# Optimization experiments

Measured on AMD Instinct MI355X. Metric: run time of the kernel, lower is better.

## Reference

```python
import jax, jax.numpy as jnp
import numpy as np

B, NB, D, H = 16384, 3, 1024, 8
HD = D // H
EPS = 1e-5

def setup_inputs() -> dict:
    key = jax.random.key(0)
    ks = jax.random.split(key, 24)
    w = lambda k, shp: jax.random.normal(k, shp, jnp.float32) * 0.02
    return {
        "x": jax.random.normal(ks[0], (B, NB, D), jnp.float32),
        # nn.MultiheadAttention params
        "in_proj_w": w(ks[1], (3 * D, D)),
        "in_proj_b": jnp.zeros((3 * D,), jnp.float32),
        "out_w": w(ks[2], (D, D)),
        "out_b": jnp.zeros((D,), jnp.float32),
        # weight_generator MLP
        "wg1_w": w(ks[3], (D, D * NB)), "wg1_b": jnp.zeros((D,), jnp.float32),
        "wg2_w": w(ks[4], (D // 2, D)), "wg2_b": jnp.zeros((D // 2,), jnp.float32),
        "wg3_w": w(ks[5], (NB, D // 2)), "wg3_b": jnp.zeros((NB,), jnp.float32),
        # refiner MLP + LayerNorms
        "r1_w": w(ks[6], (2 * D, D)), "r1_b": jnp.zeros((2 * D,), jnp.float32),
        "ln1_g": jnp.ones((2 * D,), jnp.float32), "ln1_b": jnp.zeros((2 * D,), jnp.float32),
        "r2_w": w(ks[7], (D, 2 * D)), "r2_b": jnp.zeros((D,), jnp.float32),
        "ln2_g": jnp.ones((D,), jnp.float32), "ln2_b": jnp.zeros((D,), jnp.float32),
    }

def _layernorm(x, g, b):
    m = jnp.mean(x, axis=-1, keepdims=True)
    v = jnp.mean(jnp.square(x - m), axis=-1, keepdims=True)
    return (x - m) * jax.lax.rsqrt(v + EPS) * g + b

def _forward(x, in_proj_w, in_proj_b, out_w, out_b,
             wg1_w, wg1_b, wg2_w, wg2_b, wg3_w, wg3_b,
             r1_w, r1_b, ln1_g, ln1_b, r2_w, r2_b, ln2_g, ln2_b):
    b = x.shape[0]
    # --- cross (self) attention over the NB branch tokens ---
    qkv = jnp.einsum("bsd,ed->bse", x, in_proj_w) + in_proj_b  # [B, NB, 3D]
    q, k, v = jnp.split(qkv, 3, axis=-1)
    q = q.reshape(b, NB, H, HD)
    k = k.reshape(b, NB, H, HD)
    v = v.reshape(b, NB, H, HD)
    scores = jnp.einsum("bqhd,bkhd->bhqk", q, k) / jnp.sqrt(jnp.float32(HD))
    attn = jax.nn.softmax(scores, axis=-1)
    o = jnp.einsum("bhqk,bkhd->bqhd", attn, v).reshape(b, NB, D)
    attended = jnp.einsum("bsd,ed->bse", o, out_w) + out_b  # [B, NB, D]
    # --- dynamic softmax gate over branches ---
    flat = attended.reshape(b, NB * D)
    h = jax.nn.relu(flat @ wg1_w.T + wg1_b)
    h = jax.nn.relu(h @ wg2_w.T + wg2_b)
    weights = jax.nn.softmax(h @ wg3_w.T + wg3_b, axis=-1)  # [B, NB]
    weighted = jnp.einsum("bsd,bs->bd", attended, weights)  # [B, D]
    # --- refiner (dropout inactive in eval) ---
    h = weighted @ r1_w.T + r1_b
    h = jax.nn.relu(_layernorm(h, ln1_g, ln1_b))
    out = h @ r2_w.T + r2_b
    return _layernorm(out, ln2_g, ln2_b)

def reference(x, in_proj_w, in_proj_b, out_w, out_b,
              wg1_w, wg1_b, wg2_w, wg2_b, wg3_w, wg3_b,
              r1_w, r1_b, ln1_g, ln1_b, r2_w, r2_b, ln2_g, ln2_b):
    return _forward(x, in_proj_w, in_proj_b, out_w, out_b,
                    wg1_w, wg1_b, wg2_w, wg2_b, wg3_w, wg3_b,
                    r1_w, r1_b, ln1_g, ln1_b, r2_w, r2_b, ln2_g, ln2_b)
```

## Files before the change

### kernel.cpp

```cpp
#include <hip/hip_runtime.h>
#include <hip/hip_bf16.h>

#define BB   16384
#define NBR  3
#define DD   1024
#define HH   8
#define HDD  128

typedef __attribute__((ext_vector_type(8))) short short8;
typedef __attribute__((ext_vector_type(4))) float f32x4;

__device__ __forceinline__ float b2f(ushort u) {
    union { unsigned int i; float f; } x; x.i = ((unsigned int)u) << 16; return x.f;
}
__device__ __forceinline__ ushort f2b(float f) {
    union { __hip_bfloat16 h; ushort u; } x; x.h = __float2bfloat16(f); return x.u;
}

__global__ __launch_bounds__(256) void cvt_f32_bf16(const float* __restrict__ in,
                                                    ushort* __restrict__ out, long n) {
    long i = ((long)blockIdx.x * 256 + threadIdx.x) * 4;
    if (i + 4 > n) return;
    float4 v = *reinterpret_cast<const float4*>(in + i);
    unsigned int a = ((unsigned int)f2b(v.x)) | (((unsigned int)f2b(v.y)) << 16);
    unsigned int b = ((unsigned int)f2b(v.z)) | (((unsigned int)f2b(v.w)) << 16);
    uint2 p; p.x = a; p.y = b;
    *reinterpret_cast<uint2*>(out + i) = p;
}

template<int EPI>
__global__ __launch_bounds__(512, 2)
void gemm256(const ushort* __restrict__ A, const ushort* __restrict__ Bt,
             const float* __restrict__ bias, void* __restrict__ Cout,
             int M, int N, int K) {
    extern __shared__ ushort lds[];

    const int tid  = threadIdx.x;
    const int wid  = tid >> 6;
    const int lane = tid & 63;
    const int cpx  = gridDim.x >> 3;
    const int bid  = (blockIdx.x & 7) * cpx + (blockIdx.x >> 3);
    const int nbn  = N >> 8;
    const int bm   = bid / nbn;
    const int bn   = bid % nbn;
    const long m0  = (long)bm * 256;
    const long n0  = (long)bn * 256;
    const int NT   = K >> 6;

    const int srow = tid >> 3;
    const int kel  = (((tid & 7) ^ (srow & 7)) << 3);
    const int widEl = wid * 512;

    const ushort* gA[2][2];
    const ushort* gB[2][2];
    #pragma unroll
    for (int c = 0; c < 2; c++)
        #pragma unroll
        for (int j = 0; j < 2; j++) {
            gA[c][j] = A  + (size_t)(m0 + c * 128 + j * 64 + srow) * K + kel;
            gB[c][j] = Bt + (size_t)(n0 + c * 128 + j * 64 + srow) * K + kel;
        }

    const int wr = wid >> 2, wc = wid & 3;
    const int lm15 = lane & 15;
    int aoff[8];
    #pragma unroll
    for (int m = 0; m < 8; m++) aoff[m] = (wr * 128 + m * 16 + lm15) * 64;
    int boff[4];
    #pragma unroll
    for (int c = 0; c < 4; c++) boff[c] = (wc * 64 + c * 16 + lm15) * 64;
    const int kbr[2] = {
        (((0 << 6) | ((lane >> 4) << 4)) ^ ((lane & 7) << 4)) >> 1,
        (((1 << 6) | ((lane >> 4) << 4)) ^ ((lane & 7) << 4)) >> 1
    };

    f32x4 acc[8][4];
    #pragma unroll
    for (int m = 0; m < 8; m++)
        #pragma unroll
        for (int c = 0; c < 4; c++) { f32x4 z = {0.f, 0.f, 0.f, 0.f}; acc[m][c] = z; }

    short8 af[8], bf[2];

#define STAGE(C, PB, TT) { \
    const ushort* _g0; const ushort* _g1; int _b; \
    if ((C) < 2) { _g0 = gA[(C)][0] + (TT) * 64; _g1 = gA[(C)][1] + (TT) * 64; \
                   _b = (PB) * 16384 + (C) * 8192 + widEl; } \
    else         { _g0 = gB[(C) - 2][0] + (TT) * 64; _g1 = gB[(C) - 2][1] + (TT) * 64; \
                   _b = 32768 + (PB) * 16384 + ((C) - 2) * 8192 + widEl; } \
    __builtin_amdgcn_global_load_lds((const __attribute__((address_space(1))) void*)_g0, \
        (__attribute__((address_space(3))) void*)&lds[_b], 16, 0, 0); \
    __builtin_amdgcn_global_load_lds((const __attribute__((address_space(1))) void*)_g1, \
        (__attribute__((address_space(3))) void*)&lds[_b + 4096], 16, 0, 0); }

#define READ_A(P, KK) { \
    _Pragma("unroll") \
    for (int _m = 0; _m < 8; _m++) \
        af[_m] = *(const short8*)&lds[(P) * 16384 + aoff[_m] + kbr[KK]]; }

#define READ_B2(P, KK, C0) { \
    bf[0] = *(const short8*)&lds[32768 + (P) * 16384 + boff[(C0)] + kbr[KK]]; \
    bf[1] = *(const short8*)&lds[32768 + (P) * 16384 + boff[(C0) + 1] + kbr[KK]]; }

#define MFMA8x2(C0) { \
    _Pragma("unroll") \
    for (int _m = 0; _m < 8; _m++) { \
        acc[_m][(C0)]     = __builtin_amdgcn_mfma_f32_16x16x32_bf16(af[_m], bf[0], acc[_m][(C0)], 0, 0, 0); \
        acc[_m][(C0) + 1] = __builtin_amdgcn_mfma_f32_16x16x32_bf16(af[_m], bf[1], acc[_m][(C0) + 1], 0, 0, 0); } }

#define TILE_STEP(P, T, PRE) { \
     \
    if (PRE) STAGE(0, (P) ^ 1, (T) + 1); \
    if (PRE) { asm volatile("s_waitcnt vmcnt(2)" ::: "memory"); } \
    else     { asm volatile("s_waitcnt vmcnt(0)" ::: "memory"); } \
    __builtin_amdgcn_s_barrier(); \
    asm volatile("" ::: "memory"); \
    __builtin_amdgcn_sched_barrier(0); \
    READ_A(P, 0); \
    READ_B2(P, 0, 0); \
    __builtin_amdgcn_s_setprio(1); MFMA8x2(0); __builtin_amdgcn_s_setprio(0); \
    __builtin_amdgcn_s_barrier(); \
     \
    if (PRE) STAGE(1, (P) ^ 1, (T) + 1); \
    READ_B2(P, 0, 2); \
    __builtin_amdgcn_s_barrier(); \
    __builtin_amdgcn_s_setprio(1); MFMA8x2(2); __builtin_amdgcn_s_setprio(0); \
    __builtin_amdgcn_s_barrier(); \
     \
    if (PRE) STAGE(2, (P) ^ 1, (T) + 1); \
    READ_A(P, 1); \
    READ_B2(P, 1, 0); \
    __builtin_amdgcn_s_barrier(); \
    __builtin_amdgcn_s_setprio(1); MFMA8x2(0); __builtin_amdgcn_s_setprio(0); \
    __builtin_amdgcn_s_barrier(); \
     \
    if (PRE) STAGE(3, (P) ^ 1, (T) + 1); \
    READ_B2(P, 1, 2); \
    __builtin_amdgcn_s_barrier(); \
    __builtin_amdgcn_s_setprio(1); MFMA8x2(2); __builtin_amdgcn_s_setprio(0); \
    __builtin_amdgcn_s_barrier(); }

    STAGE(0, 0, 0); STAGE(1, 0, 0); STAGE(2, 0, 0); STAGE(3, 0, 0);

    int t = 0;
    for (; t + 2 < NT; t += 2) {
        TILE_STEP(0, t, true);
        TILE_STEP(1, t + 1, true);
    }
    TILE_STEP(0, t, true);
    TILE_STEP(1, t + 1, false);

#undef TILE_STEP
#undef MFMA8x2
#undef READ_B2
#undef READ_A
#undef STAGE

    const int l16 = lane >> 4;
    #pragma unroll
    for (int c = 0; c < 4; c++) {
        const long col = n0 + wc * 64 + c * 16 + lm15;
        const float bc = bias[col];
        #pragma unroll
        for (int m = 0; m < 8; m++) {
            const long row = m0 + wr * 128 + m * 16 + l16 * 4;
            #pragma unroll
            for (int j = 0; j < 4; j++) {
                float v = acc[m][c][j] + bc;
                if (EPI == 1) v = v > 0.f ? v : 0.f;
                if (EPI == 2) ((float*)Cout)[(row + j) * (long)N + col] = v;
                else          ((ushort*)Cout)[(row + j) * (long)N + col] = f2b(v);
            }
        }
    }
}

template<int EPI>
__global__ __launch_bounds__(256, 2)
void gemm_bt(const ushort* __restrict__ A, const ushort* __restrict__ Bt,
             const float* __restrict__ bias, void* __restrict__ Cout,
             int M, int N, int K) {
    __shared__ ushort As[128 * 64];
    __shared__ ushort Bs[128 * 64];
    const int tid  = threadIdx.x;
    const int wid  = tid >> 6;
    const int lane = tid & 63;
    const int cpx  = gridDim.x >> 3;
    const int bid  = (blockIdx.x & 7) * cpx + (blockIdx.x >> 3);
    const int nbn  = N >> 7;
    const int bm   = bid / nbn;
    const int bn   = bid % nbn;
    const long m0  = (long)bm * 128;
    const long n0  = (long)bn * 128;

    const int srow = tid >> 3;
    const int scol = (tid & 7) << 3;
    const ushort* gA = A  + (m0 + srow) * (long)K + scol;
    const ushort* gB = Bt + (n0 + srow) * (long)K + scol;

    f32x4 acc[4][4];
    #pragma unroll
    for (int i = 0; i < 4; i++)
        #pragma unroll
        for (int j = 0; j < 4; j++) { f32x4 z = {0.f, 0.f, 0.f, 0.f}; acc[i][j] = z; }

    const int wr = wid >> 1, wc = wid & 1;
    const int kits = K >> 6;

    for (int kt = 0; kt < kits; ++kt) {
        const ushort* pA = gA + kt * 64;
        const ushort* pB = gB + kt * 64;
        #pragma unroll
        for (int i = 0; i < 4; i++) {
            __builtin_amdgcn_global_load_lds(
                (const __attribute__((address_space(1))) void*)(pA + (long)i * 32 * K),
                (__attribute__((address_space(3))) void*)&As[(i * 32 + wid * 8) * 64],
                16, 0, 0);
        }
        #pragma unroll
        for (int i = 0; i < 4; i++) {
            __builtin_amdgcn_global_load_lds(
                (const __attribute__((address_space(1))) void*)(pB + (long)i * 32 * K),
                (__attribute__((address_space(3))) void*)&Bs[(i * 32 + wid * 8) * 64],
                16, 0, 0);
        }
        __syncthreads();
        #pragma unroll
        for (int kk = 0; kk < 2; kk++) {
            const int ko = kk * 32 + (lane >> 4) * 8;
            short8 af[4], bf[4];
            #pragma unroll
            for (int m = 0; m < 4; m++)
                af[m] = *(const short8*)&As[(wr * 64 + m * 16 + (lane & 15)) * 64 + ko];
            #pragma unroll
            for (int n = 0; n < 4; n++)
                bf[n] = *(const short8*)&Bs[(wc * 64 + n * 16 + (lane & 15)) * 64 + ko];
            #pragma unroll
            for (int m = 0; m < 4; m++)
                #pragma unroll
                for (int n = 0; n < 4; n++)
                    acc[m][n] = __builtin_amdgcn_mfma_f32_16x16x32_bf16(af[m], bf[n], acc[m][n], 0, 0, 0);
        }
        __syncthreads();
    }

    #pragma unroll
    for (int n = 0; n < 4; n++) {
        const long c = n0 + wc * 64 + n * 16 + (lane & 15);
        const float bc = bias[c];
        #pragma unroll
        for (int m = 0; m < 4; m++) {
            const long r = m0 + wr * 64 + m * 16 + (lane >> 4) * 4;
            #pragma unroll
            for (int j = 0; j < 4; j++) {
                float v = acc[m][n][j] + bc;
                if (EPI == 1) v = v > 0.f ? v : 0.f;
                if (EPI == 2) ((float*)Cout)[(r + j) * (long)N + c] = v;
                else          ((ushort*)Cout)[(r + j) * (long)N + c] = f2b(v);
            }
        }
    }
}

__global__ __launch_bounds__(256) void attn_kernel(const ushort* __restrict__ qkv,
                                                   ushort* __restrict__ o) {
    const int w    = (blockIdx.x * 256 + threadIdx.x) >> 6;
    const int lane = threadIdx.x & 63;
    const int b = w >> 3, h = w & 7;
    const ushort* base = qkv + (size_t)b * (3 * 3072) + h * HDD + lane * 2;

    float q[3][2], k[3][2], v[3][2];
    #pragma unroll
    for (int i = 0; i < 3; i++) {
        unsigned int qu = *(const unsigned int*)(base + i * 3072);
        unsigned int ku = *(const unsigned int*)(base + i * 3072 + 1024);
        unsigned int vu = *(const unsigned int*)(base + i * 3072 + 2048);
        q[i][0] = b2f((ushort)(qu & 0xffff)); q[i][1] = b2f((ushort)(qu >> 16));
        k[i][0] = b2f((ushort)(ku & 0xffff)); k[i][1] = b2f((ushort)(ku >> 16));
        v[i][0] = b2f((ushort)(vu & 0xffff)); v[i][1] = b2f((ushort)(vu >> 16));
    }

    float s[3][3];
    #pragma unroll
    for (int i = 0; i < 3; i++)
        #pragma unroll
        for (int j = 0; j < 3; j++)
            s[i][j] = q[i][0] * k[j][0] + q[i][1] * k[j][1];

    #pragma unroll
    for (int off = 32; off; off >>= 1)
        #pragma unroll
        for (int i = 0; i < 3; i++)
            #pragma unroll
            for (int j = 0; j < 3; j++)
                s[i][j] += __shfl_xor(s[i][j], off, 64);

    const float sc = 0.08838834764831845f;
    float a[3][3];
    #pragma unroll
    for (int i = 0; i < 3; i++) {
        float l0 = s[i][0] * sc, l1 = s[i][1] * sc, l2 = s[i][2] * sc;
        float mx = fmaxf(fmaxf(l0, l1), l2);
        float e0 = __expf(l0 - mx), e1 = __expf(l1 - mx), e2 = __expf(l2 - mx);
        float inv = 1.f / (e0 + e1 + e2);
        a[i][0] = e0 * inv; a[i][1] = e1 * inv; a[i][2] = e2 * inv;
    }

    ushort* ob = o + (size_t)b * 3072 + h * HDD + lane * 2;
    #pragma unroll
    for (int i = 0; i < 3; i++) {
        float o0 = a[i][0] * v[0][0] + a[i][1] * v[1][0] + a[i][2] * v[2][0];
        float o1 = a[i][0] * v[0][1] + a[i][1] * v[1][1] + a[i][2] * v[2][1];
        unsigned int pk = ((unsigned int)f2b(o0)) | (((unsigned int)f2b(o1)) << 16);
        *(unsigned int*)(ob + i * 1024) = pk;
    }
}

__global__ __launch_bounds__(256) void gate_kernel(const ushort* __restrict__ h2,
                                                   const float* __restrict__ w3,
                                                   const float* __restrict__ b3,
                                                   const ushort* __restrict__ att,
                                                   ushort* __restrict__ weighted) {
    const int gw = (blockIdx.x * 256 + threadIdx.x) >> 6;
    const int lane = threadIdx.x & 63;
    if (gw >= BB) return;

    const ushort* hr = h2 + (size_t)gw * 512 + lane * 8;
    short8 hv = *(const short8*)hr;
    float hf[8];
    #pragma unroll
    for (int d = 0; d < 8; d++) hf[d] = b2f((ushort)hv[d]);

    float dot[3];
    #pragma unroll
    for (int s = 0; s < 3; s++) {
        const float* wr = w3 + s * 512 + lane * 8;
        float4 wa = *(const float4*)wr;
        float4 wb = *(const float4*)(wr + 4);
        dot[s] = hf[0] * wa.x + hf[1] * wa.y + hf[2] * wa.z + hf[3] * wa.w
               + hf[4] * wb.x + hf[5] * wb.y + hf[6] * wb.z + hf[7] * wb.w;
    }
    #pragma unroll
    for (int off = 32; off; off >>= 1)
        #pragma unroll
        for (int s = 0; s < 3; s++) dot[s] += __shfl_xor(dot[s], off, 64);

    float l0 = dot[0] + b3[0], l1 = dot[1] + b3[1], l2 = dot[2] + b3[2];
    float mx = fmaxf(fmaxf(l0, l1), l2);
    float e0 = __expf(l0 - mx), e1 = __expf(l1 - mx), e2 = __expf(l2 - mx);
    float inv = 1.f / (e0 + e1 + e2);
    float w0 = e0 * inv, w1 = e1 * inv, w2 = e2 * inv;

    const ushort* ab = att + (size_t)gw * 3072;
    ushort* wb = weighted + (size_t)gw * 1024;
    #pragma unroll
    for (int i = 0; i < 2; i++) {
        int d0 = (i * 64 + lane) * 8;
        short8 a0 = *(const short8*)(ab + d0);
        short8 a1 = *(const short8*)(ab + 1024 + d0);
        short8 a2 = *(const short8*)(ab + 2048 + d0);
        short8 r;
        #pragma unroll
        for (int d = 0; d < 8; d++) {
            float v = w0 * b2f((ushort)a0[d]) + w1 * b2f((ushort)a1[d]) + w2 * b2f((ushort)a2[d]);
            r[d] = (short)f2b(v);
        }
        *(short8*)(wb + d0) = r;
    }
}

template<int W, int RELU, int OUTBF16>
__global__ __launch_bounds__(256) void ln_kernel(const ushort* __restrict__ in,
                                                 const float* __restrict__ g,
                                                 const float* __restrict__ bt,
                                                 void* __restrict__ out) {
    constexpr int E = W / 256;
    const int row = blockIdx.x;
    const ushort* xr = in + (size_t)row * W + threadIdx.x * E;

    float v[E];
    if (E == 8) {
        uint4 raw = *reinterpret_cast<const uint4*>(xr);
        const unsigned int* rw = (const unsigned int*)&raw;
        #pragma unroll
        for (int p = 0; p < 4; p++) {
            v[2 * p]     = b2f((ushort)(rw[p] & 0xffff));
            v[2 * p + 1] = b2f((ushort)(rw[p] >> 16));
        }
    } else {
        uint2 raw = *reinterpret_cast<const uint2*>(xr);
        const unsigned int* rw = (const unsigned int*)&raw;
        #pragma unroll
        for (int p = 0; p < 2; p++) {
            v[2 * p]     = b2f((ushort)(rw[p] & 0xffff));
            v[2 * p + 1] = b2f((ushort)(rw[p] >> 16));
        }
    }

    float s = 0.f;
    #pragma unroll
    for (int e = 0; e < E; e++) s += v[e];

    __shared__ float red1[4], red2[4];
    const int wid = threadIdx.x >> 6, lane = threadIdx.x & 63;
    #pragma unroll
    for (int off = 32; off; off >>= 1) s += __shfl_xor(s, off, 64);
    if (lane == 0) red1[wid] = s;
    __syncthreads();
    const float mean = (red1[0] + red1[1] + red1[2] + red1[3]) / (float)W;

    float q = 0.f;
    #pragma unroll
    for (int e = 0; e < E; e++) { float d = v[e] - mean; q += d * d; }
    #pragma unroll
    for (int off = 32; off; off >>= 1) q += __shfl_xor(q, off, 64);
    if (lane == 0) red2[wid] = q;
    __syncthreads();
    const float var = (red2[0] + red2[1] + red2[2] + red2[3]) / (float)W;
    const float rstd = rsqrtf(var + 1e-5f);

    const int c0 = threadIdx.x * E;
    float o[E];
    #pragma unroll
    for (int e = 0; e < E; e++) {
        float ov = (v[e] - mean) * rstd * g[c0 + e] + bt[c0 + e];
        if (RELU) ov = ov > 0.f ? ov : 0.f;
        o[e] = ov;
    }
    if (OUTBF16) {
        ushort* op = (ushort*)out + (size_t)row * W + c0;
        unsigned int pk[E / 2];
        #pragma unroll
        for (int p = 0; p < E / 2; p++)
            pk[p] = ((unsigned int)f2b(o[2 * p])) | (((unsigned int)f2b(o[2 * p + 1])) << 16);
        if (E == 8) *reinterpret_cast<uint4*>(op) = *(uint4*)pk;
        else        *reinterpret_cast<uint2*>(op) = *(uint2*)pk;
    } else {
        float* op = (float*)out + (size_t)row * W + c0;
        #pragma unroll
        for (int p = 0; p < E / 4; p++)
            reinterpret_cast<float4*>(op)[p] = ((float4*)o)[p];
    }
}

extern "C" void kernel_launch(void* const* d_in, const int* in_sizes, int n_in,
                              void* d_out, int out_size, void* d_ws, size_t ws_size,
                              hipStream_t stream) {
    const float* x    = (const float*)d_in[0];
    const float* ipw  = (const float*)d_in[1];
    const float* ipb  = (const float*)d_in[2];
    const float* outw = (const float*)d_in[3];
    const float* outb = (const float*)d_in[4];
    const float* wg1w = (const float*)d_in[5];
    const float* wg1b = (const float*)d_in[6];
    const float* wg2w = (const float*)d_in[7];
    const float* wg2b = (const float*)d_in[8];
    const float* wg3w = (const float*)d_in[9];
    const float* wg3b = (const float*)d_in[10];
    const float* r1w  = (const float*)d_in[11];
    const float* r1b  = (const float*)d_in[12];
    const float* ln1g = (const float*)d_in[13];
    const float* ln1b = (const float*)d_in[14];
    const float* r2w  = (const float*)d_in[15];
    const float* r2b  = (const float*)d_in[16];
    const float* ln2g = (const float*)d_in[17];
    const float* ln2b = (const float*)d_in[18];

    char* ws = (char*)d_ws;
    ushort* w_ip  = (ushort*)(ws + 0);
    ushort* w_out = (ushort*)(ws + 6291456);
    ushort* w_g1  = (ushort*)(ws + 8388608);
    ushort* w_g2  = (ushort*)(ws + 14680064);
    ushort* w_r1  = (ushort*)(ws + 15728640);
    ushort* w_r2  = (ushort*)(ws + 19922944);
    char* R1 = ws + 24117248;
    char* R2 = ws + 124780544;

    ushort* xb       = (ushort*)R1;
    ushort* qkv      = (ushort*)R2;
    ushort* o_att    = (ushort*)R1;
    ushort* attended = (ushort*)R2;
    ushort* h1       = (ushort*)(R2 + 100663296);
    ushort* h2       = (ushort*)(R2 + 134217728);
    ushort* weighted = (ushort*)(R2 + 150994944);
    ushort* r1out    = (ushort*)R2;
    ushort* ln1out   = (ushort*)R1;
    ushort* r2out    = (ushort*)(R2 + 184549376);

    (void)hipFuncSetAttribute((const void*)gemm256<0>, hipFuncAttributeMaxDynamicSharedMemorySize, 131072);
    (void)hipFuncSetAttribute((const void*)gemm256<1>, hipFuncAttributeMaxDynamicSharedMemorySize, 131072);
    (void)hipFuncSetAttribute((const void*)gemm256<2>, hipFuncAttributeMaxDynamicSharedMemorySize, 131072);

    cvt_f32_bf16<<<49152, 256, 0, stream>>>(x,    xb,   (long)49152 * 1024);
    cvt_f32_bf16<<<3072,  256, 0, stream>>>(ipw,  w_ip, (long)3072 * 1024);
    cvt_f32_bf16<<<1024,  256, 0, stream>>>(outw, w_out,(long)1024 * 1024);
    cvt_f32_bf16<<<3072,  256, 0, stream>>>(wg1w, w_g1, (long)1024 * 3072);
    cvt_f32_bf16<<<512,   256, 0, stream>>>(wg2w, w_g2, (long)512 * 1024);
    cvt_f32_bf16<<<2048,  256, 0, stream>>>(r1w,  w_r1, (long)2048 * 1024);
    cvt_f32_bf16<<<2048,  256, 0, stream>>>(r2w,  w_r2, (long)1024 * 2048);

    gemm256<0><<<192 * 12, 512, 131072, stream>>>(xb, w_ip, ipb, qkv, 49152, 3072, 1024);
    attn_kernel<<<32768, 256, 0, stream>>>(qkv, o_att);
    gemm256<0><<<192 * 4,  512, 131072, stream>>>(o_att, w_out, outb, attended, 49152, 1024, 1024);
    gemm256<1><<<64 * 4,   512, 131072, stream>>>(attended, w_g1, wg1b, h1, 16384, 1024, 3072);
    gemm_bt<1><<<128 * 4, 256, 0, stream>>>(h1, w_g2, wg2b, h2, 16384, 512, 1024);
    gate_kernel<<<4096, 256, 0, stream>>>(h2, wg3w, wg3b, attended, weighted);
    gemm256<0><<<64 * 8,   512, 131072, stream>>>(weighted, w_r1, r1b, r1out, 16384, 2048, 1024);
    ln_kernel<2048, 1, 1><<<16384, 256, 0, stream>>>(r1out, ln1g, ln1b, ln1out);
    gemm256<0><<<64 * 4,   512, 131072, stream>>>(ln1out, w_r2, r2b, r2out, 16384, 1024, 2048);
    ln_kernel<1024, 0, 0><<<16384, 256, 0, stream>>>(r2out, ln2g, ln2b, d_out);
}
```

Baseline: 921.8 us.

## Fold out-projection into gate MLP weights and apply it after branch weighting

Uses linearity of the attention out-projection to precompute a fused weight (gate layer-1 weight times out_w) and fused bias, so the gate MLP reads the raw attention outputs directly. The branch-weighted sum is taken over attention outputs and out_w is applied once per batch row instead of per branch token, removing the largest out-projection GEMM. Adds a small transpose, a weight-product GEMM and a bias reduction per call, and changes bf16 rounding order.

```diff
diff --git a/kernel.cpp b/kernel.cpp
--- a/kernel.cpp
+++ b/kernel.cpp
@@ -26,6 +26,35 @@
     unsigned int b = ((unsigned int)f2b(v.z)) | (((unsigned int)f2b(v.w)) << 16);
     uint2 p; p.x = a; p.y = b;
     *reinterpret_cast<uint2*>(out + i) = p;
+}
+
+__global__ __launch_bounds__(256) void transpose_cvt(const float* __restrict__ in,
+                                                     ushort* __restrict__ out) {
+    __shared__ float t[32][33];
+    const int bx = blockIdx.x & 31, by = blockIdx.x >> 5;
+    const int tx = threadIdx.x & 31, ty = threadIdx.x >> 5;
+    #pragma unroll
+    for (int i = 0; i < 4; i++)
+        t[ty + i * 8][tx] = in[(size_t)(by * 32 + ty + i * 8) * 1024 + bx * 32 + tx];
+    __syncthreads();
+    #pragma unroll
+    for (int i = 0; i < 4; i++)
+        out[(size_t)(bx * 32 + ty + i * 8) * 1024 + by * 32 + tx] = f2b(t[tx][ty + i * 8]);
+}
+
+__global__ __launch_bounds__(256) void bias1_kernel(const float* __restrict__ wg1w,
+                                                    const float* __restrict__ wg1b,
+                                                    const float* __restrict__ outb,
+                                                    float* __restrict__ b1p) {
+    const int o = (blockIdx.x * 256 + threadIdx.x) >> 6;
+    const int lane = threadIdx.x & 63;
+    const float* wr = wg1w + (size_t)o * 3072;
+    float s = 0.f;
+    for (int e = lane; e < 1024; e += 64)
+        s += outb[e] * (wr[e] + wr[e + 1024] + wr[e + 2048]);
+    #pragma unroll
+    for (int off = 32; off; off >>= 1) s += __shfl_xor(s, off, 64);
+    if (lane == 0) b1p[o] = s + wg1b[o];
 }
 
 template<int EPI>
@@ -179,7 +208,7 @@
 __global__ __launch_bounds__(256, 2)
 void gemm_bt(const ushort* __restrict__ A, const ushort* __restrict__ Bt,
              const float* __restrict__ bias, void* __restrict__ Cout,
-             int M, int N, int K) {
+             int M, int N, int K, int lda, int ldb, int ldc, int sA, int sC) {
     __shared__ ushort As[128 * 64];
     __shared__ ushort Bs[128 * 64];
     const int tid  = threadIdx.x;
@@ -193,10 +222,13 @@
     const long m0  = (long)bm * 128;
     const long n0  = (long)bn * 128;
 
+    A += (size_t)blockIdx.y * sA;
+    const long cOff = (long)blockIdx.y * sC;
+
     const int srow = tid >> 3;
     const int scol = (tid & 7) << 3;
-    const ushort* gA = A  + (m0 + srow) * (long)K + scol;
-    const ushort* gB = Bt + (n0 + srow) * (long)K + scol;
+    const ushort* gA = A  + (m0 + srow) * (long)lda + scol;
+    const ushort* gB = Bt + (n0 + srow) * (long)ldb + scol;
 
     f32x4 acc[4][4];
     #pragma unroll
@@ -213,14 +245,14 @@
         #pragma unroll
         for (int i = 0; i < 4; i++) {
             __builtin_amdgcn_global_load_lds(
-                (const __attribute__((address_space(1))) void*)(pA + (long)i * 32 * K),
+                (const __attribute__((address_space(1))) void*)(pA + (long)i * 32 * lda),
                 (__attribute__((address_space(3))) void*)&As[(i * 32 + wid * 8) * 64],
                 16, 0, 0);
         }
         #pragma unroll
         for (int i = 0; i < 4; i++) {
             __builtin_amdgcn_global_load_lds(
-                (const __attribute__((address_space(1))) void*)(pB + (long)i * 32 * K),
+                (const __attribute__((address_space(1))) void*)(pB + (long)i * 32 * ldb),
                 (__attribute__((address_space(3))) void*)&Bs[(i * 32 + wid * 8) * 64],
                 16, 0, 0);
         }
@@ -255,8 +287,8 @@
             for (int j = 0; j < 4; j++) {
                 float v = acc[m][n][j] + bc;
                 if (EPI == 1) v = v > 0.f ? v : 0.f;
-                if (EPI == 2) ((float*)Cout)[(r + j) * (long)N + c] = v;
-                else          ((ushort*)Cout)[(r + j) * (long)N + c] = f2b(v);
+                if (EPI == 2) ((float*)Cout)[(r + j) * (long)ldc + cOff + c] = v;
+                else          ((ushort*)Cout)[(r + j) * (long)ldc + cOff + c] = f2b(v);
             }
         }
     }
@@ -479,13 +511,17 @@
     ushort* xb       = (ushort*)R1;
     ushort* qkv      = (ushort*)R2;
     ushort* o_att    = (ushort*)R1;
-    ushort* attended = (ushort*)R2;
-    ushort* h1       = (ushort*)(R2 + 100663296);
-    ushort* h2       = (ushort*)(R2 + 134217728);
-    ushort* weighted = (ushort*)(R2 + 150994944);
-    ushort* r1out    = (ushort*)R2;
+    ushort* h1       = (ushort*)(R2 + 0);
+    ushort* h2       = (ushort*)(R2 + 33554432);
+    ushort* wsum_o   = (ushort*)(R2 + 50331648);
+    ushort* weighted = (ushort*)(R2 + 83886080);
+    ushort* r1out    = (ushort*)(R2 + 117440512);
+    ushort* r2out    = (ushort*)(R2 + 184549376);
+    ushort* w1p      = (ushort*)(R2 + 218103808);
+    ushort* w_outT   = (ushort*)(R2 + 224395264);
+    float*  b1p      = (float*) (R2 + 226492416);
+    float*  zbias    = (float*) (R2 + 226496512);
     ushort* ln1out   = (ushort*)R1;
-    ushort* r2out    = (ushort*)(R2 + 184549376);
 
     (void)hipFuncSetAttribute((const void*)gemm256<0>, hipFuncAttributeMaxDynamicSharedMemorySize, 131072);
     (void)hipFuncSetAttribute((const void*)gemm256<1>, hipFuncAttributeMaxDynamicSharedMemorySize, 131072);
@@ -501,12 +537,22 @@
 
     gemm256<0><<<192 * 12, 512, 131072, stream>>>(xb, w_ip, ipb, qkv, 49152, 3072, 1024);
     attn_kernel<<<32768, 256, 0, stream>>>(qkv, o_att);
-    gemm256<0><<<192 * 4,  512, 131072, stream>>>(o_att, w_out, outb, attended, 49152, 1024, 1024);
-    gemm256<1><<<64 * 4,   512, 131072, stream>>>(attended, w_g1, wg1b, h1, 16384, 1024, 3072);
-    gemm_bt<1><<<128 * 4, 256, 0, stream>>>(h1, w_g2, wg2b, h2, 16384, 512, 1024);
-    gate_kernel<<<4096, 256, 0, stream>>>(h2, wg3w, wg3b, attended, weighted);
-    gemm256<0><<<64 * 8,   512, 131072, stream>>>(weighted, w_r1, r1b, r1out, 16384, 2048, 1024);
+
+    (void)hipMemsetAsync(zbias, 0, 4096, stream);
+    transpose_cvt<<<1024, 256, 0, stream>>>(outw, w_outT);
+    gemm_bt<0><<<dim3(64, 3), 256, 0, stream>>>(w_g1, w_outT, zbias, w1p,
+                                                1024, 1024, 1024, 3072, 1024, 3072, 1024, 1024);
+    bias1_kernel<<<256, 256, 0, stream>>>(wg1w, wg1b, outb, b1p);
+
+    gemm256<1><<<64 * 4, 512, 131072, stream>>>(o_att, w1p, b1p, h1, 16384, 1024, 3072);
+    gemm_bt<1><<<dim3(128 * 4, 1), 256, 0, stream>>>(h1, w_g2, wg2b, h2,
+                                                     16384, 512, 1024, 1024, 1024, 512, 0, 0);
+    gate_kernel<<<4096, 256, 0, stream>>>(h2, wg3w, wg3b, o_att, wsum_o);
+
+    gemm256<0><<<64 * 4, 512, 131072, stream>>>(wsum_o, w_out, outb, weighted, 16384, 1024, 1024);
+
+    gemm256<0><<<64 * 8, 512, 131072, stream>>>(weighted, w_r1, r1b, r1out, 16384, 2048, 1024);
     ln_kernel<2048, 1, 1><<<16384, 256, 0, stream>>>(r1out, ln1g, ln1b, ln1out);
-    gemm256<0><<<64 * 4,   512, 131072, stream>>>(ln1out, w_r2, r2b, r2out, 16384, 1024, 2048);
+    gemm256<0><<<64 * 4, 512, 131072, stream>>>(ln1out, w_r2, r2b, r2out, 16384, 1024, 2048);
     ln_kernel<1024, 0, 0><<<16384, 256, 0, stream>>>(r2out, ln2g, ln2b, d_out);
 }
```

New measurement: 885.9 us. 3.9% less time.
